# Kernel tuning notes

Hardware: AMD Instinct MI355X
Metric: run time of the kernel (lower is better)

Reference implementation:

```python
import jax, jax.numpy as jnp
import numpy as np
import math

D_MODEL = 1024
N_HEAD = 16
D_HEAD = D_MODEL // N_HEAD
SCALE = math.sqrt(D_HEAD)
B, S = 8, 512


def setup_inputs() -> dict:
    key = jax.random.key(0)
    ks = jax.random.split(key, 7)
    x = jax.random.normal(ks[0], (B, S, D_MODEL), dtype=jnp.float32)
    mask = jnp.ones((B, S), dtype=jnp.int32)
    qmask = jax.random.randint(ks[1], (B, S), 0, 2).astype(jnp.int32)
    # params
    Wqkv = jax.random.normal(ks[2], (4 * D_MODEL, D_MODEL), dtype=jnp.float32) / math.sqrt(D_MODEL)
    fc_w = jax.random.normal(ks[3], (D_MODEL, D_MODEL), dtype=jnp.float32) / math.sqrt(D_MODEL)
    fc_b = jnp.zeros((D_MODEL,), dtype=jnp.float32)
    shift = jnp.abs(jax.random.normal(ks[4], (1,), dtype=jnp.float32)) + 0.001
    bias = -jnp.abs(jax.random.normal(ks[5], (1,), dtype=jnp.float32))
    return {"x": x, "mask": mask, "qmask": qmask, "Wqkv": Wqkv,
            "fc_w": fc_w, "fc_b": fc_b, "shift": shift, "bias": bias}


def reference(x, mask, qmask, Wqkv, fc_w, fc_b, shift, bias):
    Bsz, L, D = x.shape
    qkv = x @ Wqkv.T  # [B,S,4D], no bias
    q, k1, k2, v = jnp.split(qkv, 4, axis=-1)

    def heads(t):  # [B,S,D] -> [B,H,S,dh]
        return t.reshape(Bsz, L, N_HEAD, D_HEAD).transpose(0, 2, 1, 3)

    q, k1, k2, v = heads(q), heads(k1), heads(k2), heads(v)

    attn_self = jnp.einsum('bhqd,bhkd->bhqk', q, k1)
    attn_others = jnp.einsum('bhqd,bhkd->bhqk', q, k2)
    same_spk = (qmask[:, :, None] == qmask[:, None, :])[:, None]  # [B,1,S,S]
    attn = jnp.where(same_spk, attn_self, attn_others) / SCALE

    # key padding mask
    attn = jnp.where((mask == 0)[:, None, None, :], -jnp.inf, attn)

    # Gaussian distance bias: -(shift*(i-j)^2 + bias)
    pos = jnp.arange(L, dtype=jnp.float32)
    sq_dist = (pos[:, None] - pos[None, :]) ** 2  # [S,S]
    attn = attn - (shift[0] * sq_dist + bias[0])

    p = jax.nn.softmax(attn, axis=-1)  # dropout=0 (eval)
    out = jnp.einsum('bhqk,bhkd->bhqd', p, v)
    out = out.transpose(0, 2, 1, 3).reshape(Bsz, L, D)
    return out @ fc_w.T + fc_b
```

## Files before the change

### kernel.cpp

```cpp
#include <hip/hip_runtime.h>

typedef unsigned short u16;
typedef __bf16 bf16_t;
typedef bf16_t bf16x8 __attribute__((ext_vector_type(8)));
typedef float f32x4 __attribute__((ext_vector_type(4)));
typedef u16 u16x8 __attribute__((ext_vector_type(8)));
typedef u16 u16x4 __attribute__((ext_vector_type(4)));

__device__ __forceinline__ u16 f2b(float f) {
    unsigned int u = __float_as_uint(f);
    u += 0x7fffu + ((u >> 16) & 1u);
    return (u16)(u >> 16);
}

__device__ __forceinline__ f32x4 mfma16(u16x8 a, u16x8 b, f32x4 c) {
    return __builtin_amdgcn_mfma_f32_16x16x32_bf16(
        __builtin_bit_cast(bf16x8, a), __builtin_bit_cast(bf16x8, b), c, 0, 0, 0);
}

#define GLDS16(gp, lp)                                                          \
    __builtin_amdgcn_global_load_lds(                                           \
        (const __attribute__((address_space(1))) void*)(gp),                    \
        (__attribute__((address_space(3))) void*)(lp), 16, 0, 0)

__global__ __launch_bounds__(256) void cvt3_kernel(const float* __restrict__ s0,
                                                   const float* __restrict__ s1,
                                                   const float* __restrict__ s2,
                                                   u16* __restrict__ d0,
                                                   u16* __restrict__ d1,
                                                   u16* __restrict__ d2) {
    int i = (blockIdx.x * 256 + threadIdx.x) * 4;
    const float* src; u16* dst;
    if (i < 4194304)       { src = s0;           dst = d0;           }
    else if (i < 8388608)  { src = s1 - 4194304; dst = d1 - 4194304; }
    else                   { src = s2 - 8388608; dst = d2 - 8388608; }
    float4 f = *(const float4*)(src + i);
    u16x4 o = { f2b(f.x), f2b(f.y), f2b(f.z), f2b(f.w) };
    *(u16x4*)(dst + i) = o;
}

__global__ __launch_bounds__(512, 2) void gemm256_qkv(
    const u16* __restrict__ A, const u16* __restrict__ Bw,
    u16* __restrict__ Qf, u16* __restrict__ K1f,
    u16* __restrict__ K2f, u16* __restrict__ Vf)
{
    __shared__ u16 lds[4][2][8192];

    const int t = threadIdx.x;
    const int lane = t & 63;
    const int w = t >> 6;
    const int wm = w >> 2, wn = w & 3;
    const int lr = lane & 15, quad = lane >> 4;

    const int lin = blockIdx.x;
    const int swz = (lin & 7) * 32 + (lin >> 3);
    const int bx = swz & 15, by = swz >> 4;
    const int tileM = by * 256, tileN = bx * 256;

    const int srow = t >> 2;
    const int scol = ((t & 3) ^ ((t >> 3) & 3)) * 8;
    const u16* Asrc0 = A + (size_t)(tileM + srow) * 1024 + scol;
    const u16* Asrc1 = Asrc0 + (size_t)128 * 1024;
    const u16* Bsrc0 = Bw + (size_t)(tileN + srow) * 1024 + scol;
    const u16* Bsrc1 = Bsrc0 + (size_t)128 * 1024;

    const int swzq = (quad ^ ((lr >> 1) & 3)) * 8;
    const int aoff = (wm * 128 + lr) * 32 + swzq;
    const int boff = (wn * 64 + lr) * 32 + swzq;

    f32x4 acc[8][4] = {};

#define STAGE_A(tk, buf)                                                        \
    do { GLDS16(Asrc0 + (tk) * 32, &lds[buf][0][t * 8]);                        \
         GLDS16(Asrc1 + (tk) * 32, &lds[buf][0][(t + 512) * 8]); } while (0)
#define STAGE_B(tk, buf)                                                        \
    do { GLDS16(Bsrc0 + (tk) * 32, &lds[buf][1][t * 8]);                        \
         GLDS16(Bsrc1 + (tk) * 32, &lds[buf][1][(t + 512) * 8]); } while (0)

#define DO_TILE(tk, DO_ST, VMASM)                                               \
    do {                                                                        \
        const int cur_ = (tk) & 3, nxt_ = ((tk) + 3) & 3;                       \
        const u16* aL = &lds[cur_][0][0];                                       \
        const u16* bL = &lds[cur_][1][0];                                       \
        if (DO_ST) { STAGE_A((tk) + 3, nxt_); STAGE_B((tk) + 3, nxt_); }        \
        u16x8 af[8], bf[4];                                                     \
        _Pragma("unroll") for (int i = 0; i < 4; ++i)                           \
            bf[i] = *(const u16x8*)(bL + boff + i * 512);                       \
        _Pragma("unroll") for (int i = 0; i < 8; ++i)                           \
            af[i] = *(const u16x8*)(aL + aoff + i * 512);                       \
        __builtin_amdgcn_s_setprio(1);                                          \
        _Pragma("unroll") for (int mi = 0; mi < 8; ++mi)                        \
            _Pragma("unroll") for (int ni = 0; ni < 4; ++ni)                    \
                acc[mi][ni] = mfma16(af[mi], bf[ni], acc[mi][ni]);              \
        __builtin_amdgcn_s_setprio(0);                                          \
        VMASM;                                                                  \
        __builtin_amdgcn_s_barrier();                                           \
    } while (0)

    STAGE_A(0, 0); STAGE_B(0, 0);
    STAGE_A(1, 1); STAGE_B(1, 1);
    STAGE_A(2, 2); STAGE_B(2, 2);
    asm volatile("s_waitcnt vmcnt(8)" ::: "memory");
    __builtin_amdgcn_s_barrier();

#pragma unroll 4
    for (int tk = 0; tk < 28; ++tk)
        DO_TILE(tk, true, asm volatile("s_waitcnt vmcnt(8)" ::: "memory"));
    DO_TILE(28, true,  asm volatile("s_waitcnt vmcnt(8)" ::: "memory"));
    DO_TILE(29, false, asm volatile("s_waitcnt vmcnt(4)" ::: "memory"));
    DO_TILE(30, false, asm volatile("s_waitcnt vmcnt(0)" ::: "memory"));
    DO_TILE(31, false, (void)0);
#undef DO_TILE
#undef STAGE_A
#undef STAGE_B

    const int kv = tileN >> 10;
    const int h  = ((tileN + wn * 64) >> 6) & 15;
    const int bh = (((tileM + wm * 128) >> 9) << 4) + h;
    const int M16 = ((tileM & 511) + wm * 128) >> 4;
    const int M32 = M16 >> 1;

    if (kv < 3) {
        u16* base = (kv == 0) ? Qf : (kv == 1) ? K1f : K2f;
#pragma unroll
        for (int mi = 0; mi < 8; ++mi)
#pragma unroll
            for (int ni = 0; ni < 4; ++ni) {
                size_t idx0 = ((size_t)((bh * 32 + M16 + mi) * 2 + (ni >> 1))) * 512
                            + (((ni * 2 + (lr >> 3)) & 3) * 16 + quad * 4) * 8 + (lr & 7);
#pragma unroll
                for (int r = 0; r < 4; ++r)
                    base[idx0 + r * 8] = f2b(acc[mi][ni][r]);
            }
    } else {
#pragma unroll
        for (int mi = 0; mi < 8; ++mi)
#pragma unroll
            for (int ni = 0; ni < 4; ++ni) {
                size_t idx = ((size_t)((bh * 4 + ni) * 16 + M32 + (mi >> 1))) * 512
                           + (((mi * 2 + (quad >> 1)) & 3) * 16 + lr) * 8 + (quad & 1) * 4;
                u16x4 o = { f2b(acc[mi][ni][0]), f2b(acc[mi][ni][1]),
                            f2b(acc[mi][ni][2]), f2b(acc[mi][ni][3]) };
                *(u16x4*)(Vf + idx) = o;
            }
    }
}

__global__ __launch_bounds__(256, 2) void gemm128_proj(
    const u16* __restrict__ A, const u16* __restrict__ Bw,
    float* __restrict__ Cf, const float* __restrict__ biasp)
{
    __shared__ u16 lds[4][2][4096];

    const int t = threadIdx.x;
    const int lane = t & 63;
    const int w = t >> 6;
    const int wm = w >> 1, wn = w & 1;
    const int lr = lane & 15, quad = lane >> 4;

    const int lin = blockIdx.x;
    const int xcd = lin & 7, j = lin >> 3;
    const int bx = j & 7;
    const int by = xcd * 4 + (j >> 3);
    const int tileM = by * 128, tileN = bx * 128;

    const int scol = ((t & 3) ^ ((t >> 3) & 3)) * 8;
    const u16* Asrc0 = A + (size_t)(tileM + (t >> 2)) * 1024 + scol;
    const u16* Asrc1 = Asrc0 + (size_t)64 * 1024;
    const u16* Bsrc0 = Bw + (size_t)(tileN + (t >> 2)) * 1024 + scol;
    const u16* Bsrc1 = Bsrc0 + (size_t)64 * 1024;

    const int swzq = (quad ^ ((lr >> 1) & 3)) * 8;
    const int aoff = (wm * 64 + lr) * 32 + swzq;
    const int boff = (wn * 64 + lr) * 32 + swzq;

    f32x4 acc[4][4] = {};

#define STAGE_A(tk, buf)                                                        \
    do { GLDS16(Asrc0 + (tk) * 32, &lds[buf][0][t * 8]);                        \
         GLDS16(Asrc1 + (tk) * 32, &lds[buf][0][(t + 256) * 8]); } while (0)
#define STAGE_B(tk, buf)                                                        \
    do { GLDS16(Bsrc0 + (tk) * 32, &lds[buf][1][t * 8]);                        \
         GLDS16(Bsrc1 + (tk) * 32, &lds[buf][1][(t + 256) * 8]); } while (0)

#define DO_TILE(tk, DO_ST, VMASM)                                               \
    do {                                                                        \
        const int cur_ = (tk) & 3, nxt_ = ((tk) + 3) & 3;                       \
        const u16* aL = &lds[cur_][0][0];                                       \
        const u16* bL = &lds[cur_][1][0];                                       \
        if (DO_ST) { STAGE_A((tk) + 3, nxt_); STAGE_B((tk) + 3, nxt_); }        \
        u16x8 af[4], bf[4];                                                     \
        _Pragma("unroll") for (int i = 0; i < 4; ++i)                           \
            af[i] = *(const u16x8*)(aL + aoff + i * 512);                       \
        _Pragma("unroll") for (int i = 0; i < 4; ++i)                           \
            bf[i] = *(const u16x8*)(bL + boff + i * 512);                       \
        __builtin_amdgcn_s_setprio(1);                                          \
        _Pragma("unroll") for (int mi = 0; mi < 4; ++mi)                        \
            _Pragma("unroll") for (int ni = 0; ni < 4; ++ni)                    \
                acc[mi][ni] = mfma16(af[mi], bf[ni], acc[mi][ni]);              \
        __builtin_amdgcn_s_setprio(0);                                          \
        VMASM;                                                                  \
        __builtin_amdgcn_s_barrier();                                           \
    } while (0)

    STAGE_A(0, 0); STAGE_B(0, 0);
    STAGE_A(1, 1); STAGE_B(1, 1);
    STAGE_A(2, 2); STAGE_B(2, 2);
    asm volatile("s_waitcnt vmcnt(8)" ::: "memory");
    __builtin_amdgcn_s_barrier();

#pragma unroll 4
    for (int tk = 0; tk < 28; ++tk)
        DO_TILE(tk, true, asm volatile("s_waitcnt vmcnt(8)" ::: "memory"));
    DO_TILE(28, true,  asm volatile("s_waitcnt vmcnt(8)" ::: "memory"));
    DO_TILE(29, false, asm volatile("s_waitcnt vmcnt(4)" ::: "memory"));
    DO_TILE(30, false, asm volatile("s_waitcnt vmcnt(0)" ::: "memory"));
    DO_TILE(31, false, (void)0);
#undef DO_TILE
#undef STAGE_A
#undef STAGE_B

#pragma unroll
    for (int mi = 0; mi < 4; ++mi)
#pragma unroll
        for (int ni = 0; ni < 4; ++ni) {
            int n = tileN + wn * 64 + ni * 16 + lr;
            float bv = biasp[n];
#pragma unroll
            for (int r = 0; r < 4; ++r) {
                int m = tileM + wm * 64 + mi * 16 + quad * 4 + r;
                Cf[(size_t)m * 1024 + n] = acc[mi][ni][r] + bv;
            }
        }
}

__global__ __launch_bounds__(256, 2) void attn_kernel(
    const u16* __restrict__ qfm, const u16* __restrict__ k1fm,
    const u16* __restrict__ k2fm, const u16* __restrict__ vfm,
    const int* __restrict__ maskp, const int* __restrict__ qmaskp,
    const float* __restrict__ shiftp, const float* __restrict__ biasp,
    u16* __restrict__ ao)
{
    __shared__ u16 Ks[2][2][2][2][512];
    __shared__ u16 Vs[2][4][512];
    __shared__ u16 Pw[4][2][512];

    const int bh = blockIdx.x & 127, qh = blockIdx.x >> 7;
    const int b = bh >> 4;
    const int t = threadIdx.x, lane = t & 63, w = t >> 6;
    const int lr = lane & 15, quad = lane >> 4;
    const float shiftv = shiftp[0], biasv = biasp[0];

    const int m16a = qh * 8 + w;
    const int m16b = m16a + 4;
    const int qbaseA = m16a * 16;
    const int qbaseB = m16b * 16;

    const u16* qsrcA = qfm + ((size_t)(bh * 32 + m16a) * 2) * 512 + lane * 8;
    const u16* qsrcB = qfm + ((size_t)(bh * 32 + m16b) * 2) * 512 + lane * 8;
    u16x8 qa0 = *(const u16x8*)(qsrcA);
    u16x8 qa1 = *(const u16x8*)(qsrcA + 512);
    u16x8 qb0 = *(const u16x8*)(qsrcB);
    u16x8 qb1 = *(const u16x8*)(qsrcB + 512);

    int qmrA[4], qmrB[4]; float rowfA[4], rowfB[4];
#pragma unroll
    for (int r = 0; r < 4; ++r) {
        int ma = qbaseA + quad * 4 + r;
        int mb = qbaseB + quad * 4 + r;
        qmrA[r] = qmaskp[b * 512 + ma];
        qmrB[r] = qmaskp[b * 512 + mb];
        rowfA[r] = (float)ma;
        rowfB[r] = (float)mb;
    }

    f32x4 oa0 = {0,0,0,0}, oa1 = {0,0,0,0}, oa2 = {0,0,0,0}, oa3 = {0,0,0,0};
    f32x4 ob0 = {0,0,0,0}, ob1 = {0,0,0,0}, ob2 = {0,0,0,0}, ob3 = {0,0,0,0};
    float lsa[4] = {0,0,0,0}, lsb[4] = {0,0,0,0};

    u16* pbA = &Pw[w][0][0];
    u16* pbB = &Pw[w][1][0];
    const int wa0 = quad * 128 + (((lr >> 3) ^ quad) * 8) + (lr & 7);
    const int wa1 = quad * 128 + (((2 | (lr >> 3)) ^ quad) * 8) + (lr & 7);
    const int ra = lr * 32 + ((quad ^ (lr >> 2)) * 8);

    const int s_ = w >> 1, kh_ = w & 1;
    const u16* k1s = k1fm + ((size_t)(bh * 32 + s_) * 2 + kh_) * 512 + lane * 8;
    const u16* k2s = k2fm + ((size_t)(bh * 32 + s_) * 2 + kh_) * 512 + lane * 8;
    const u16* vsrc = vfm + ((size_t)(bh * 4 + w) * 16) * 512 + lane * 8;

#define ASTAGE(cc, bufi)                                                        \
    do {                                                                        \
        GLDS16(k1s + (size_t)(cc) * 2048, &Ks[bufi][0][s_][kh_][lane * 8]);     \
        GLDS16(k2s + (size_t)(cc) * 2048, &Ks[bufi][1][s_][kh_][lane * 8]);     \
        GLDS16(vsrc + (size_t)(cc) * 512, &Vs[bufi][w][lane * 8]);              \
    } while (0)

    const int* qmb = qmaskp + b * 512;
    const int* kmb = maskp + b * 512;

    ASTAGE(0, 0);
    __syncthreads();

    for (int cc = 0; cc < 16; ++cc) {
        const int cur = cc & 1;
        if (cc < 15) ASTAGE(cc + 1, cur ^ 1);

        u16x8 k1t0a = *(const u16x8*)(&Ks[cur][0][0][0][lane * 8]);
        u16x8 k1t0b = *(const u16x8*)(&Ks[cur][0][0][1][lane * 8]);
        u16x8 k1t1a = *(const u16x8*)(&Ks[cur][0][1][0][lane * 8]);
        u16x8 k1t1b = *(const u16x8*)(&Ks[cur][0][1][1][lane * 8]);
        u16x8 k2t0a = *(const u16x8*)(&Ks[cur][1][0][0][lane * 8]);
        u16x8 k2t0b = *(const u16x8*)(&Ks[cur][1][0][1][lane * 8]);
        u16x8 k2t1a = *(const u16x8*)(&Ks[cur][1][1][0][lane * 8]);
        u16x8 k2t1b = *(const u16x8*)(&Ks[cur][1][1][1][lane * 8]);

        f32x4 z = {0.f, 0.f, 0.f, 0.f};
        f32x4 sa1t0 = mfma16(qa1, k1t0b, mfma16(qa0, k1t0a, z));
        f32x4 sa2t0 = mfma16(qa1, k2t0b, mfma16(qa0, k2t0a, z));
        f32x4 sa1t1 = mfma16(qa1, k1t1b, mfma16(qa0, k1t1a, z));
        f32x4 sa2t1 = mfma16(qa1, k2t1b, mfma16(qa0, k2t1a, z));
        f32x4 sb1t0 = mfma16(qb1, k1t0b, mfma16(qb0, k1t0a, z));
        f32x4 sb2t0 = mfma16(qb1, k2t0b, mfma16(qb0, k2t0a, z));
        f32x4 sb1t1 = mfma16(qb1, k1t1b, mfma16(qb0, k1t1a, z));
        f32x4 sb2t1 = mfma16(qb1, k2t1b, mfma16(qb0, k2t1a, z));

        const int col0 = cc * 32 + lr, col1 = col0 + 16;
        const int qmc0 = qmb[col0], qmc1 = qmb[col1];
        const float ka0 = (kmb[col0] ? 0.f : -1e30f) - 10.0f;
        const float ka1 = (kmb[col1] ? 0.f : -1e30f) - 10.0f;
        const float colf0 = (float)col0, colf1 = (float)col1;

        u16x8 vf0 = *(const u16x8*)(&Vs[cur][0][lane * 8]);
        u16x8 vf1 = *(const u16x8*)(&Vs[cur][1][lane * 8]);
        u16x8 vf2 = *(const u16x8*)(&Vs[cur][2][lane * 8]);
        u16x8 vf3 = *(const u16x8*)(&Vs[cur][3][lane * 8]);

        {
            float p0[4], p1[4];
#pragma unroll
            for (int r = 0; r < 4; ++r) {
                float d0 = rowfA[r] - colf0;
                float d1 = rowfA[r] - colf1;
                float sel0 = (qmrA[r] == qmc0) ? sa1t0[r] : sa2t0[r];
                float sel1 = (qmrA[r] == qmc1) ? sa1t1[r] : sa2t1[r];
                float v0 = fmaf(sel0, 0.125f, -fmaf(shiftv * d0, d0, biasv)) + ka0;
                float v1 = fmaf(sel1, 0.125f, -fmaf(shiftv * d1, d1, biasv)) + ka1;
                p0[r] = __expf(v0);
                p1[r] = __expf(v1);
                lsa[r] += p0[r] + p1[r];
            }
#pragma unroll
            for (int r = 0; r < 4; ++r) {
                pbA[wa0 + r * 32] = f2b(p0[r]);
                pbA[wa1 + r * 32] = f2b(p1[r]);
            }
            u16x8 af = *(const u16x8*)(pbA + ra);
            oa0 = mfma16(af, vf0, oa0);
            oa1 = mfma16(af, vf1, oa1);
            oa2 = mfma16(af, vf2, oa2);
            oa3 = mfma16(af, vf3, oa3);
        }
        {
            float p0[4], p1[4];
#pragma unroll
            for (int r = 0; r < 4; ++r) {
                float d0 = rowfB[r] - colf0;
                float d1 = rowfB[r] - colf1;
                float sel0 = (qmrB[r] == qmc0) ? sb1t0[r] : sb2t0[r];
                float sel1 = (qmrB[r] == qmc1) ? sb1t1[r] : sb2t1[r];
                float v0 = fmaf(sel0, 0.125f, -fmaf(shiftv * d0, d0, biasv)) + ka0;
                float v1 = fmaf(sel1, 0.125f, -fmaf(shiftv * d1, d1, biasv)) + ka1;
                p0[r] = __expf(v0);
                p1[r] = __expf(v1);
                lsb[r] += p0[r] + p1[r];
            }
#pragma unroll
            for (int r = 0; r < 4; ++r) {
                pbB[wa0 + r * 32] = f2b(p0[r]);
                pbB[wa1 + r * 32] = f2b(p1[r]);
            }
            u16x8 af = *(const u16x8*)(pbB + ra);
            ob0 = mfma16(af, vf0, ob0);
            ob1 = mfma16(af, vf1, ob1);
            ob2 = mfma16(af, vf2, ob2);
            ob3 = mfma16(af, vf3, ob3);
        }

        __syncthreads();
    }
#undef ASTAGE

#pragma unroll
    for (int r = 0; r < 4; ++r) {
        float s = lsa[r];
#pragma unroll
        for (int m = 1; m < 16; m <<= 1) s += __shfl_xor(s, m);
        float inv = 1.0f / s;
        int grow = b * 512 + qbaseA + quad * 4 + r;
        u16* orow = ao + (size_t)grow * 1024 + (bh & 15) * 64 + lr;
        orow[0]  = f2b(oa0[r] * inv);
        orow[16] = f2b(oa1[r] * inv);
        orow[32] = f2b(oa2[r] * inv);
        orow[48] = f2b(oa3[r] * inv);
    }
#pragma unroll
    for (int r = 0; r < 4; ++r) {
        float s = lsb[r];
#pragma unroll
        for (int m = 1; m < 16; m <<= 1) s += __shfl_xor(s, m);
        float inv = 1.0f / s;
        int grow = b * 512 + qbaseB + quad * 4 + r;
        u16* orow = ao + (size_t)grow * 1024 + (bh & 15) * 64 + lr;
        orow[0]  = f2b(ob0[r] * inv);
        orow[16] = f2b(ob1[r] * inv);
        orow[32] = f2b(ob2[r] * inv);
        orow[48] = f2b(ob3[r] * inv);
    }
}

extern "C" void kernel_launch(void* const* d_in, const int* in_sizes, int n_in,
                              void* d_out, int out_size, void* d_ws, size_t ws_size,
                              hipStream_t stream) {
    (void)in_sizes; (void)n_in; (void)out_size; (void)ws_size;
    const float* x      = (const float*)d_in[0];
    const int*   maskp  = (const int*)d_in[1];
    const int*   qmaskp = (const int*)d_in[2];
    const float* Wqkv   = (const float*)d_in[3];
    const float* fc_w   = (const float*)d_in[4];
    const float* fc_b   = (const float*)d_in[5];
    const float* shiftp = (const float*)d_in[6];
    const float* biasp  = (const float*)d_in[7];
    float* out = (float*)d_out;

    char* ws = (char*)d_ws;
    u16* xb   = (u16*)(ws);
    u16* wb   = (u16*)(ws + (8u << 20));
    u16* fwb  = (u16*)(ws + (16u << 20));
    u16* qfm  = (u16*)(ws + (18u << 20));
    u16* k1fm = (u16*)(ws + (26u << 20));
    u16* k2fm = (u16*)(ws + (34u << 20));
    u16* vfm  = (u16*)(ws + (42u << 20));
    u16* aob  = (u16*)(ws + (50u << 20));

    cvt3_kernel<<<9216, 256, 0, stream>>>(x, Wqkv, fc_w, xb, wb, fwb);
    gemm256_qkv<<<256, 512, 0, stream>>>(xb, wb, qfm, k1fm, k2fm, vfm);
    attn_kernel<<<512, 256, 0, stream>>>(qfm, k1fm, k2fm, vfm, maskp, qmaskp,
                                         shiftp, biasp, aob);
    gemm128_proj<<<256, 256, 0, stream>>>(aob, fwb, out, fc_b);
}
```

Measured before the change: 175.2 us.

## Retile QKV GEMM to 256x128 blocks with register double-buffered LDS reads

After: 184.3 us. 1.05x slower.

```diff
diff --git a/kernel.cpp b/kernel.cpp
--- a/kernel.cpp
+++ b/kernel.cpp
@@ -39,111 +39,121 @@
     *(u16x4*)(dst + i) = o;
 }
 
-__global__ __launch_bounds__(512, 2) void gemm256_qkv(
+__global__ __launch_bounds__(256, 1) void gemm256x128_qkv(
     const u16* __restrict__ A, const u16* __restrict__ Bw,
     u16* __restrict__ Qf, u16* __restrict__ K1f,
     u16* __restrict__ K2f, u16* __restrict__ Vf)
 {
-    __shared__ u16 lds[4][2][8192];
+    __shared__ u16 lds[4][12288];
 
     const int t = threadIdx.x;
     const int lane = t & 63;
     const int w = t >> 6;
-    const int wm = w >> 2, wn = w & 3;
+    const int wm = w >> 1, wn = w & 1;
     const int lr = lane & 15, quad = lane >> 4;
 
     const int lin = blockIdx.x;
-    const int swz = (lin & 7) * 32 + (lin >> 3);
-    const int bx = swz & 15, by = swz >> 4;
-    const int tileM = by * 256, tileN = bx * 256;
-
-    const int srow = t >> 2;
+    const int xcd = lin & 7, j = lin >> 3;
+    const int bx = (xcd & 3) * 8 + (j & 7);
+    const int by = (xcd >> 2) * 8 + (j >> 3);
+    const int tileM = by * 256, tileN = bx * 128;
+
     const int scol = ((t & 3) ^ ((t >> 3) & 3)) * 8;
-    const u16* Asrc0 = A + (size_t)(tileM + srow) * 1024 + scol;
-    const u16* Asrc1 = Asrc0 + (size_t)128 * 1024;
-    const u16* Bsrc0 = Bw + (size_t)(tileN + srow) * 1024 + scol;
-    const u16* Bsrc1 = Bsrc0 + (size_t)128 * 1024;
+    const u16* Asrc = A + (size_t)(tileM + (t >> 2)) * 1024 + scol;
+    const u16* Bsrc = Bw + (size_t)(tileN + (t >> 2)) * 1024 + scol;
 
     const int swzq = (quad ^ ((lr >> 1) & 3)) * 8;
     const int aoff = (wm * 128 + lr) * 32 + swzq;
     const int boff = (wn * 64 + lr) * 32 + swzq;
 
     f32x4 acc[8][4] = {};
-
-#define STAGE_A(tk, buf)                                                        \
-    do { GLDS16(Asrc0 + (tk) * 32, &lds[buf][0][t * 8]);                        \
-         GLDS16(Asrc1 + (tk) * 32, &lds[buf][0][(t + 512) * 8]); } while (0)
-#define STAGE_B(tk, buf)                                                        \
-    do { GLDS16(Bsrc0 + (tk) * 32, &lds[buf][1][t * 8]);                        \
-         GLDS16(Bsrc1 + (tk) * 32, &lds[buf][1][(t + 512) * 8]); } while (0)
-
-#define DO_TILE(tk, DO_ST, VMASM)                                               \
-    do {                                                                        \
-        const int cur_ = (tk) & 3, nxt_ = ((tk) + 3) & 3;                       \
-        const u16* aL = &lds[cur_][0][0];                                       \
-        const u16* bL = &lds[cur_][1][0];                                       \
-        if (DO_ST) { STAGE_A((tk) + 3, nxt_); STAGE_B((tk) + 3, nxt_); }        \
-        u16x8 af[8], bf[4];                                                     \
+    u16x8 afA[8], bfA[4], afB[8], bfB[4];
+
+#define STAGE(tk, buf)                                                          \
+    do {                                                                        \
+        GLDS16(Asrc + (tk) * 32,                       &lds[buf][t * 8]);       \
+        GLDS16(Asrc + (size_t) 64 * 1024 + (tk) * 32,  &lds[buf][(t + 256) * 8]); \
+        GLDS16(Asrc + (size_t)128 * 1024 + (tk) * 32,  &lds[buf][(t + 512) * 8]); \
+        GLDS16(Asrc + (size_t)192 * 1024 + (tk) * 32,  &lds[buf][(t + 768) * 8]); \
+        GLDS16(Bsrc + (tk) * 32,                       &lds[buf][8192 + t * 8]); \
+        GLDS16(Bsrc + (size_t) 64 * 1024 + (tk) * 32,  &lds[buf][8192 + (t + 256) * 8]); \
+    } while (0)
+
+#define RD(tk, af_, bf_)                                                        \
+    do {                                                                        \
+        const u16* aL = &lds[(tk) & 3][0];                                      \
+        const u16* bL = &lds[(tk) & 3][8192];                                   \
+        _Pragma("unroll") for (int i = 0; i < 8; ++i)                           \
+            af_[i] = *(const u16x8*)(aL + aoff + i * 512);                      \
         _Pragma("unroll") for (int i = 0; i < 4; ++i)                           \
-            bf[i] = *(const u16x8*)(bL + boff + i * 512);                       \
-        _Pragma("unroll") for (int i = 0; i < 8; ++i)                           \
-            af[i] = *(const u16x8*)(aL + aoff + i * 512);                       \
+            bf_[i] = *(const u16x8*)(bL + boff + i * 512);                      \
+    } while (0)
+
+#define MM(af_, bf_)                                                            \
+    do {                                                                        \
         __builtin_amdgcn_s_setprio(1);                                          \
         _Pragma("unroll") for (int mi = 0; mi < 8; ++mi)                        \
             _Pragma("unroll") for (int ni = 0; ni < 4; ++ni)                    \
-                acc[mi][ni] = mfma16(af[mi], bf[ni], acc[mi][ni]);              \
+                acc[mi][ni] = mfma16(af_[mi], bf_[ni], acc[mi][ni]);            \
         __builtin_amdgcn_s_setprio(0);                                          \
+    } while (0)
+
+#define DO_TILE(tk, afc, bfc, afn, bfn, DO_ST, DO_RD, VMASM)                    \
+    do {                                                                        \
+        if (DO_ST) STAGE((tk) + 3, ((tk) + 3) & 3);                             \
+        if (DO_RD) RD((tk) + 1, afn, bfn);                                      \
+        MM(afc, bfc);                                                           \
         VMASM;                                                                  \
         __builtin_amdgcn_s_barrier();                                           \
     } while (0)
 
-    STAGE_A(0, 0); STAGE_B(0, 0);
-    STAGE_A(1, 1); STAGE_B(1, 1);
-    STAGE_A(2, 2); STAGE_B(2, 2);
-    asm volatile("s_waitcnt vmcnt(8)" ::: "memory");
+    STAGE(0, 0); STAGE(1, 1); STAGE(2, 2);
+    asm volatile("s_waitcnt vmcnt(6)" ::: "memory");
     __builtin_amdgcn_s_barrier();
-
-#pragma unroll 4
-    for (int tk = 0; tk < 28; ++tk)
-        DO_TILE(tk, true, asm volatile("s_waitcnt vmcnt(8)" ::: "memory"));
-    DO_TILE(28, true,  asm volatile("s_waitcnt vmcnt(8)" ::: "memory"));
-    DO_TILE(29, false, asm volatile("s_waitcnt vmcnt(4)" ::: "memory"));
-    DO_TILE(30, false, asm volatile("s_waitcnt vmcnt(0)" ::: "memory"));
-    DO_TILE(31, false, (void)0);
+    RD(0, afA, bfA);
+
+#pragma unroll
+    for (int jj = 0; jj < 14; ++jj) {
+        DO_TILE(2 * jj,     afA, bfA, afB, bfB, true, true,
+                asm volatile("s_waitcnt vmcnt(6)" ::: "memory"));
+        DO_TILE(2 * jj + 1, afB, bfB, afA, bfA, true, true,
+                asm volatile("s_waitcnt vmcnt(6)" ::: "memory"));
+    }
+    DO_TILE(28, afA, bfA, afB, bfB, true,  true,
+            asm volatile("s_waitcnt vmcnt(6)" ::: "memory"));
+    DO_TILE(29, afB, bfB, afA, bfA, false, true,
+            asm volatile("s_waitcnt vmcnt(0)" ::: "memory"));
+    DO_TILE(30, afA, bfA, afB, bfB, false, true,  (void)0);
+    DO_TILE(31, afB, bfB, afA, bfA, false, false, (void)0);
 #undef DO_TILE
-#undef STAGE_A
-#undef STAGE_B
-
-    const int kv = tileN >> 10;
-    const int h  = ((tileN + wn * 64) >> 6) & 15;
-    const int bh = (((tileM + wm * 128) >> 9) << 4) + h;
-    const int M16 = ((tileM & 511) + wm * 128) >> 4;
-    const int M32 = M16 >> 1;
-
-    if (kv < 3) {
-        u16* base = (kv == 0) ? Qf : (kv == 1) ? K1f : K2f;
-#pragma unroll
-        for (int mi = 0; mi < 8; ++mi)
-#pragma unroll
-            for (int ni = 0; ni < 4; ++ni) {
-                size_t idx0 = ((size_t)((bh * 32 + M16 + mi) * 2 + (ni >> 1))) * 512
-                            + (((ni * 2 + (lr >> 3)) & 3) * 16 + quad * 4) * 8 + (lr & 7);
-#pragma unroll
-                for (int r = 0; r < 4; ++r)
-                    base[idx0 + r * 8] = f2b(acc[mi][ni][r]);
-            }
-    } else {
-#pragma unroll
-        for (int mi = 0; mi < 8; ++mi)
-#pragma unroll
-            for (int ni = 0; ni < 4; ++ni) {
-                size_t idx = ((size_t)((bh * 4 + ni) * 16 + M32 + (mi >> 1))) * 512
-                           + (((mi * 2 + (quad >> 1)) & 3) * 16 + lr) * 8 + (quad & 1) * 4;
-                u16x4 o = { f2b(acc[mi][ni][0]), f2b(acc[mi][ni][1]),
-                            f2b(acc[mi][ni][2]), f2b(acc[mi][ni][3]) };
-                *(u16x4*)(Vf + idx) = o;
-            }
-    }
+#undef MM
+#undef RD
+#undef STAGE
+
+#pragma unroll
+    for (int mi = 0; mi < 8; ++mi)
+#pragma unroll
+        for (int ni = 0; ni < 4; ++ni) {
+            int n = tileN + wn * 64 + ni * 16 + lr;
+            int kv = n >> 10;
+            int h = (n >> 6) & 15, d = n & 63;
+#pragma unroll
+            for (int r = 0; r < 4; ++r) {
+                int m = tileM + wm * 128 + mi * 16 + quad * 4 + r;
+                int s = m & 511, bh = ((m >> 9) << 4) + h;
+                u16 v = f2b(acc[mi][ni][r]);
+                if (kv < 3) {
+                    u16* base = (kv == 0) ? Qf : (kv == 1) ? K1f : K2f;
+                    size_t idx = ((size_t)((bh * 32 + (s >> 4)) * 2 + (d >> 5))) * 512
+                               + (((d >> 3) & 3) * 16 + (s & 15)) * 8 + (d & 7);
+                    base[idx] = v;
+                } else {
+                    size_t idx = ((size_t)((bh * 4 + (d >> 4)) * 16 + (s >> 5))) * 512
+                               + (((s >> 3) & 3) * 16 + (d & 15)) * 8 + (s & 7);
+                    Vf[idx] = v;
+                }
+            }
+        }
 }
 
 __global__ __launch_bounds__(256, 2) void gemm128_proj(
@@ -444,7 +454,7 @@
     u16* aob  = (u16*)(ws + (50u << 20));
 
     cvt3_kernel<<<9216, 256, 0, stream>>>(x, Wqkv, fc_w, xb, wb, fwb);
-    gemm256_qkv<<<256, 512, 0, stream>>>(xb, wb, qfm, k1fm, k2fm, vfm);
+    gemm256x128_qkv<<<512, 256, 0, stream>>>(xb, wb, qfm, k1fm, k2fm, vfm);
     attn_kernel<<<512, 256, 0, stream>>>(qfm, k1fm, k2fm, vfm, maskp, qmaskp,
                                          shiftp, biasp, aob);
     gemm128_proj<<<256, 256, 0, stream>>>(aob, fwb, out, fc_b);
```
